# Kernel tuning notes

Hardware: AMD Instinct MI355X
Metric: run time of the kernel (lower is better)

The kernel has to match this reference:

```python
import jax, jax.numpy as jnp
import numpy as np

N_NODES = 100000
N_EDGES = 1600000
D_FEAT = 48


def sage_conv(x, src, dst, Wl, Wr, b):
    # mean aggregation of neighbor messages x[src] at dst (PyG source_to_target)
    msg_sum = jax.ops.segment_sum(x[src], dst, num_segments=N_NODES)  # [N, d]
    cnt = jax.ops.segment_sum(jnp.ones((src.shape[0],), x.dtype), dst,
                              num_segments=N_NODES)  # [N]
    mean = msg_sum / jnp.maximum(cnt, 1.0)[:, None]
    # out = lin_l(mean neighbors) + lin_r(self); bias only on lin_l (PyG default)
    return mean @ Wl + b + x @ Wr


def setup_inputs() -> dict:
    key = jax.random.key(0)
    ks = jax.random.split(key, 8)
    x = jax.random.normal(ks[0], (N_NODES, D_FEAT), jnp.float32)
    edge_index = jax.random.randint(ks[1], (2, N_EDGES), 0, N_NODES, jnp.int64)
    def w(k, fi, fo):
        return jax.random.normal(k, (fi, fo), jnp.float32) / np.sqrt(fi)
    return {
        "x": x,
        "edge_index": edge_index,
        "W1l": w(ks[2], D_FEAT, 32), "W1r": w(ks[3], D_FEAT, 32),
        "b1": jnp.zeros((32,), jnp.float32),
        "W2l": w(ks[4], 32, 16), "W2r": w(ks[5], 32, 16),
        "b2": jnp.zeros((16,), jnp.float32),
        "Wlin": w(ks[6], 16, 2), "blin": jnp.zeros((2,), jnp.float32),
    }


def reference(x, edge_index, W1l, W1r, b1, W2l, W2r, b2, Wlin, blin):
    src, dst = edge_index[0], edge_index[1]
    h = jax.nn.relu(sage_conv(x, src, dst, W1l, W1r, b1))
    h = jax.nn.relu(sage_conv(h, src, dst, W2l, W2r, b2))
    return h @ Wlin + blin  # [N, 2] logits
```

## Files before the change

kernel.cpp:

```cpp
#include <hip/hip_runtime.h>
#include <hip/hip_bf16.h>


constexpr int NN  = 100000;
constexpr int NE  = 1600000;
constexpr int NCH = (NN + 255) / 256;
constexpr int NB  = 391;
constexpr int CAP = 4608;
constexpr int SEG = CAP + 3 * 256;
constexpr int T1  = 2048;
constexpr int NB1 = (NE + T1 - 1) / T1;

__device__ __forceinline__ float bl(unsigned u) { return __uint_as_float(u << 16); }
__device__ __forceinline__ float bh(unsigned u) { return __uint_as_float(u & 0xffff0000u); }
__device__ __forceinline__ unsigned f2b(float x) {
    unsigned u = __float_as_uint(x);
    return (u + 0x7fffu + ((u >> 16) & 1u)) >> 16;
}
__device__ __forceinline__ unsigned pack2(float a, float b) {
    return f2b(a) | (f2b(b) << 16);
}

__device__ __forceinline__ int wave_incl_scan(int v, int lane) {
#pragma unroll
    for (int d = 1; d < 64; d <<= 1) {
        int t = __shfl_up(v, d, 64);
        if (lane >= d) v += t;
    }
    return v;
}

__global__ __launch_bounds__(256) void k1_kernel(
    const float* __restrict__ X,
    const float* __restrict__ Wl,
    const float* __restrict__ Wr,
    const int*   __restrict__ ei,
    int* __restrict__ bsize, unsigned* __restrict__ bbuf,
    __hip_bfloat16* __restrict__ P, __hip_bfloat16* __restrict__ R)
{
    __shared__ float sW[2][48 * 32];
    __shared__ int hist[NB], base[NB];
    __shared__ int s_any;

    if (blockIdx.x < NCH) {
        for (int i = threadIdx.x; i < 48 * 32; i += 256) {
            sW[0][i] = Wl[i];
            sW[1][i] = Wr[i];
        }
        __syncthreads();
        int n = blockIdx.x * 256 + threadIdx.x;
        if (n > NN) return;
        if (n == NN) {
            uint4 z = make_uint4(0, 0, 0, 0);
            uint4* pp = reinterpret_cast<uint4*>(P + (size_t)NN * 32);
#pragma unroll
            for (int i = 0; i < 4; ++i) pp[i] = z;
            return;
        }
        float xr[48];
        const float4* xp = reinterpret_cast<const float4*>(X + (size_t)n * 48);
#pragma unroll
        for (int i = 0; i < 12; ++i) {
            float4 u = xp[i];
            xr[i*4+0] = u.x; xr[i*4+1] = u.y; xr[i*4+2] = u.z; xr[i*4+3] = u.w;
        }
        float accp[32], accr[32];
#pragma unroll
        for (int j = 0; j < 32; ++j) { accp[j] = 0.f; accr[j] = 0.f; }
#pragma unroll
        for (int k = 0; k < 48; ++k) {
            float xk = xr[k];
#pragma unroll
            for (int j = 0; j < 32; ++j) {
                accp[j] += xk * sW[0][k * 32 + j];
                accr[j] += xk * sW[1][k * 32 + j];
            }
        }
        uint4* pp = reinterpret_cast<uint4*>(P + (size_t)n * 32);
        uint4* rp = reinterpret_cast<uint4*>(R + (size_t)n * 32);
#pragma unroll
        for (int i = 0; i < 4; ++i) {
            uint4 u, v;
            u.x = pack2(accp[i*8+0], accp[i*8+1]); u.y = pack2(accp[i*8+2], accp[i*8+3]);
            u.z = pack2(accp[i*8+4], accp[i*8+5]); u.w = pack2(accp[i*8+6], accp[i*8+7]);
            v.x = pack2(accr[i*8+0], accr[i*8+1]); v.y = pack2(accr[i*8+2], accr[i*8+3]);
            v.z = pack2(accr[i*8+4], accr[i*8+5]); v.w = pack2(accr[i*8+6], accr[i*8+7]);
            pp[i] = u;
            rp[i] = v;
        }
    } else {
        if (threadIdx.x == 0) s_any = 0;
        for (int i = threadIdx.x; i < NB; i += 256) hist[i] = 0;
        __syncthreads();
        int dv = 0;
        for (int i = threadIdx.x; i < 2048; i += 256) dv |= ei[2 * i + 1];
        if (dv != 0) atomicOr(&s_any, 1);
        __syncthreads();
        const bool i64 = (s_any == 0);
        const int e0 = (blockIdx.x - NCH) * T1;

        auto sweep = [&](auto&& f) {
            if (i64) {
                const int4* sp = reinterpret_cast<const int4*>(ei) + (e0 >> 1);
                const int4* dp = reinterpret_cast<const int4*>(ei) + ((NE + e0) >> 1);
#pragma unroll
                for (int it = 0; it < 4; ++it) {
                    int p = it * 256 + threadIdx.x;
                    int e = e0 + 2 * p;
                    if (e + 2 <= NE) {
                        int4 s4 = sp[p], d4 = dp[p];
                        f(s4.x, d4.x);
                        f(s4.z, d4.z);
                    } else {
                        for (int e2 = e; e2 < NE && e2 < e + 2; ++e2)
                            f(ei[(size_t)e2 << 1], ei[(size_t)(NE + e2) << 1]);
                    }
                }
            } else {
                const int4* sp = reinterpret_cast<const int4*>(ei) + (e0 >> 2);
                const int4* dp = reinterpret_cast<const int4*>(ei) + ((NE + e0) >> 2);
#pragma unroll
                for (int it = 0; it < 2; ++it) {
                    int q = it * 256 + threadIdx.x;
                    int e = e0 + 4 * q;
                    if (e + 4 <= NE) {
                        int4 s4 = sp[q], d4 = dp[q];
                        f(s4.x, d4.x);
                        f(s4.y, d4.y);
                        f(s4.z, d4.z);
                        f(s4.w, d4.w);
                    } else {
                        for (int e2 = e; e2 < NE && e2 < e + 4; ++e2)
                            f(ei[e2], ei[NE + e2]);
                    }
                }
            }
        };

        sweep([&](int s, int d) {
            if ((unsigned)s < (unsigned)NN && (unsigned)d < (unsigned)NN)
                atomicAdd(&hist[d >> 8], 1);
        });
        __syncthreads();
        for (int b = threadIdx.x; b < NB; b += 256) {
            int h = hist[b];
            base[b] = h ? atomicAdd(&bsize[b], h) : 0;
        }
        __syncthreads();
        sweep([&](int s, int d) {
            if ((unsigned)s < (unsigned)NN && (unsigned)d < (unsigned)NN) {
                int bk = d >> 8;
                int pos = atomicAdd(&base[bk], 1);
                if (pos < CAP)
                    bbuf[(size_t)bk * CAP + pos] =
                        ((unsigned)s << 8) | (unsigned)(d & 255);
            }
        });
    }
}

__global__ __launch_bounds__(1024) void k2_kernel(
    const int* __restrict__ bsize, const unsigned* __restrict__ bbuf,
    int* __restrict__ deg, int* __restrict__ rowstart, int* __restrict__ csr_src)
{
    __shared__ int ldeg[256], lcur[256], ws[4];
    int b = blockIdx.x, t = threadIdx.x;
    int bs = b * SEG;

    int S = min(bsize[b], CAP);
    const unsigned* bp = bbuf + (size_t)b * CAP;
    if (t < 256) ldeg[t] = 0;
    __syncthreads();
    for (int i = t; i < S; i += 1024)
        atomicAdd(&ldeg[bp[i] & 255u], 1);
    __syncthreads();

    int v = 0, pv = 0, incl = 0, excl = 0;
    if (t < 256) {
        v  = ldeg[t];
        pv = (v + 3) & ~3;
        incl = wave_incl_scan(pv, t & 63);
        if ((t & 63) == 63) ws[t >> 6] = incl;
    }
    __syncthreads();
    if (t < 256) {
        int off = 0, wid = t >> 6;
#pragma unroll
        for (int w = 0; w < 3; ++w)
            if (wid > w) off += ws[w];
        excl = off + incl - pv;
        int node = (b << 8) + t;
        if (node < NN) {
            deg[node] = v;
            rowstart[node] = bs + excl;
        }
        lcur[t] = excl;
    }
    __syncthreads();

    for (int i = t; i < S; i += 1024) {
        unsigned pk = bp[i];
        int pos = atomicAdd(&lcur[pk & 255u], 1);
        csr_src[bs + pos] = (int)(pk >> 8);
    }
    if (t < 256)
        for (int p = excl + v; p < excl + pv; ++p)
            csr_src[bs + p] = NN;
}

__global__ __launch_bounds__(256) void gather1f_kernel(
    const int* __restrict__ rowstart, const int* __restrict__ deg,
    const int* __restrict__ csr_src,
    const __hip_bfloat16* __restrict__ p1,
    const __hip_bfloat16* __restrict__ r1,
    const float* __restrict__ b1,
    const float* __restrict__ W2l,
    const float* __restrict__ W2r,
    __hip_bfloat16* __restrict__ P2,
    __hip_bfloat16* __restrict__ R2)
{
    __shared__ float sW2l[32 * 16], sW2r[32 * 16], sb1[32];
    __shared__ float shh[32 * 65];
    int t = threadIdx.x;
    for (int i = t; i < 32 * 16; i += 256) { sW2l[i] = W2l[i]; sW2r[i] = W2r[i]; }
    if (t < 32) sb1[t] = b1[t];
    __syncthreads();

    int loc = t >> 2, c = t & 3;
    int n = blockIdx.x * 64 + loc;
    bool valid = n < NN;

    if (valid) {
        int start = rowstart[n], dn = deg[n];
        int pv4 = ((dn + 3) & ~3) >> 2;
        const uint4* prow = reinterpret_cast<const uint4*>(p1);
        const int4* cp4 = reinterpret_cast<const int4*>(csr_src + start);
        uint4 r = reinterpret_cast<const uint4*>(r1)[(size_t)n * 4 + c];
        float acc[8];
#pragma unroll
        for (int j = 0; j < 8; ++j) acc[j] = 0.f;
        int4 s4 = cp4[0];
        for (int k = 0; k < pv4; ++k) {
            int4 nx = cp4[k + 1];
            uint4 a = prow[(size_t)s4.x * 4 + c];
            uint4 b = prow[(size_t)s4.y * 4 + c];
            uint4 d = prow[(size_t)s4.z * 4 + c];
            uint4 e = prow[(size_t)s4.w * 4 + c];
            acc[0] += bl(a.x) + bl(b.x) + bl(d.x) + bl(e.x);
            acc[1] += bh(a.x) + bh(b.x) + bh(d.x) + bh(e.x);
            acc[2] += bl(a.y) + bl(b.y) + bl(d.y) + bl(e.y);
            acc[3] += bh(a.y) + bh(b.y) + bh(d.y) + bh(e.y);
            acc[4] += bl(a.z) + bl(b.z) + bl(d.z) + bl(e.z);
            acc[5] += bh(a.z) + bh(b.z) + bh(d.z) + bh(e.z);
            acc[6] += bl(a.w) + bl(b.w) + bl(d.w) + bl(e.w);
            acc[7] += bh(a.w) + bh(b.w) + bh(d.w) + bh(e.w);
            s4 = nx;
        }
        float inv = 1.0f / fmaxf((float)dn, 1.0f);
        float rr[8] = { bl(r.x), bh(r.x), bl(r.y), bh(r.y),
                        bl(r.z), bh(r.z), bl(r.w), bh(r.w) };
#pragma unroll
        for (int j = 0; j < 8; ++j)
            shh[(c * 8 + j) * 65 + loc] = fmaxf(acc[j] * inv + rr[j] + sb1[c * 8 + j], 0.f);
    }
    __syncthreads();

    if (valid) {
        float accp[4], accr[4];
#pragma unroll
        for (int j = 0; j < 4; ++j) { accp[j] = 0.f; accr[j] = 0.f; }
#pragma unroll
        for (int k = 0; k < 32; ++k) {
            float hk = shh[k * 65 + loc];
#pragma unroll
            for (int j = 0; j < 4; ++j) {
                accp[j] += hk * sW2l[k * 16 + c * 4 + j];
                accr[j] += hk * sW2r[k * 16 + c * 4 + j];
            }
        }
        uint2 up, ur;
        up.x = pack2(accp[0], accp[1]); up.y = pack2(accp[2], accp[3]);
        ur.x = pack2(accr[0], accr[1]); ur.y = pack2(accr[2], accr[3]);
        reinterpret_cast<uint2*>(P2)[(size_t)n * 4 + c] = up;
        reinterpret_cast<uint2*>(R2)[(size_t)n * 4 + c] = ur;
    } else if (n == NN) {
        uint2 z = make_uint2(0, 0);
        reinterpret_cast<uint2*>(P2)[(size_t)NN * 4 + c] = z;
        reinterpret_cast<uint2*>(R2)[(size_t)NN * 4 + c] = z;
    }
}

__global__ __launch_bounds__(256) void gather2_kernel(
    const int* __restrict__ rowstart, const int* __restrict__ deg,
    const int* __restrict__ csr_src,
    const __hip_bfloat16* __restrict__ P2,
    const __hip_bfloat16* __restrict__ R2,
    const float* __restrict__ b2,
    const float* __restrict__ Wlin,
    const float* __restrict__ blin,
    float* __restrict__ out)
{
    __shared__ float sb[16], sW[32], sbl[2];
    if (threadIdx.x < 16) sb[threadIdx.x] = b2[threadIdx.x];
    else if (threadIdx.x < 48) sW[threadIdx.x - 16] = Wlin[threadIdx.x - 16];
    else if (threadIdx.x < 50) sbl[threadIdx.x - 48] = blin[threadIdx.x - 48];
    __syncthreads();
    int t = blockIdx.x * 256 + threadIdx.x;
    int n = t >> 1, c = t & 1;
    if (n >= NN) return;
    int start = rowstart[n], dn = deg[n];
    int pv4 = ((dn + 3) & ~3) >> 2;

    const uint4* prow = reinterpret_cast<const uint4*>(P2);
    const int4* cp4 = reinterpret_cast<const int4*>(csr_src + start);
    uint4 r = reinterpret_cast<const uint4*>(R2)[(size_t)n * 2 + c];
    float acc[8];
#pragma unroll
    for (int j = 0; j < 8; ++j) acc[j] = 0.f;
    int4 s4 = cp4[0];
    for (int k = 0; k < pv4; ++k) {
        int4 nx = cp4[k + 1];
        uint4 a = prow[(size_t)s4.x * 2 + c];
        uint4 b = prow[(size_t)s4.y * 2 + c];
        uint4 d = prow[(size_t)s4.z * 2 + c];
        uint4 e = prow[(size_t)s4.w * 2 + c];
        acc[0] += bl(a.x) + bl(b.x) + bl(d.x) + bl(e.x);
        acc[1] += bh(a.x) + bh(b.x) + bh(d.x) + bh(e.x);
        acc[2] += bl(a.y) + bl(b.y) + bl(d.y) + bl(e.y);
        acc[3] += bh(a.y) + bh(b.y) + bh(d.y) + bh(e.y);
        acc[4] += bl(a.z) + bl(b.z) + bl(d.z) + bl(e.z);
        acc[5] += bh(a.z) + bh(b.z) + bh(d.z) + bh(e.z);
        acc[6] += bl(a.w) + bl(b.w) + bl(d.w) + bl(e.w);
        acc[7] += bh(a.w) + bh(b.w) + bh(d.w) + bh(e.w);
        s4 = nx;
    }
    float inv = 1.0f / fmaxf((float)dn, 1.0f);
    float rr[8] = { bl(r.x), bh(r.x), bl(r.y), bh(r.y),
                    bl(r.z), bh(r.z), bl(r.w), bh(r.w) };
    float o0 = 0.f, o1 = 0.f;
#pragma unroll
    for (int j = 0; j < 8; ++j) {
        int kk = c * 8 + j;
        float hv = fmaxf(acc[j] * inv + rr[j] + sb[kk], 0.f);
        o0 += hv * sW[kk * 2];
        o1 += hv * sW[kk * 2 + 1];
    }
    o0 += __shfl_xor(o0, 1, 64);
    o1 += __shfl_xor(o1, 1, 64);
    if (c == 0)
        reinterpret_cast<float2*>(out)[n] = make_float2(o0 + sbl[0], o1 + sbl[1]);
}

extern "C" void kernel_launch(void* const* d_in, const int* in_sizes, int n_in,
                              void* d_out, int out_size, void* d_ws, size_t ws_size,
                              hipStream_t stream)
{
    const float* x    = (const float*)d_in[0];
    const int*   ei   = (const int*)d_in[1];
    const float* W1l  = (const float*)d_in[2];
    const float* W1r  = (const float*)d_in[3];
    const float* b1   = (const float*)d_in[4];
    const float* W2l  = (const float*)d_in[5];
    const float* W2r  = (const float*)d_in[6];
    const float* b2   = (const float*)d_in[7];
    const float* Wlin = (const float*)d_in[8];
    const float* blin = (const float*)d_in[9];
    float* out = (float*)d_out;

    char* wsb = (char*)d_ws;
    int*      bsize    = (int*)(wsb + 64);
    int*      deg      = (int*)(wsb + 4096);
    int*      rowstart = (int*)(wsb + 404096);
    int*      csr_src  = (int*)(wsb + 804096);
    unsigned* bbuf     = (unsigned*)(wsb + 9300000);
    __hip_bfloat16* p1 = (__hip_bfloat16*)(wsb + 16600000);
    __hip_bfloat16* r1 = (__hip_bfloat16*)(wsb + 23100000);
    __hip_bfloat16* p2 = (__hip_bfloat16*)(wsb + 29600000);
    __hip_bfloat16* r2 = (__hip_bfloat16*)(wsb + 32900000);

    dim3 blk(256);

    hipMemsetAsync(bsize, 0, NB * sizeof(int), stream);
    k1_kernel<<<NCH + NB1, blk, 0, stream>>>(x, W1l, W1r, ei, bsize, bbuf, p1, r1);
    k2_kernel<<<NB, dim3(1024), 0, stream>>>(bsize, bbuf, deg, rowstart, csr_src);
    gather1f_kernel<<<(NN + 1 + 63) / 64, blk, 0, stream>>>(
        rowstart, deg, csr_src, p1, r1, b1, W2l, W2r, p2, r2);
    gather2_kernel<<<(NN * 2 + 255) / 256, blk, 0, stream>>>(
        rowstart, deg, csr_src, p2, r2, b2, Wlin, blin, out);
}
```

Before: 181.8 us.

## Replace CSR build and gathers with per-bucket LDS atomic scatter aggregation

Drops the CSR construction kernel and aggregates both layers directly from the destination-bucketed edge buffer. Each 1024-thread block owns 256 destination nodes and accumulates gathered bf16 neighbor rows into shared-memory float accumulators with LDS atomics, counting degrees the same way. This removes one kernel launch plus the csr_src/rowstart/deg global traffic, at the cost of heavy LDS atomic contention, only 391 blocks of parallelism, and a summation order that is no longer deterministic.

```diff
diff --git a/kernel.cpp b/kernel.cpp
--- a/kernel.cpp
+++ b/kernel.cpp
@@ -7,7 +7,6 @@
 constexpr int NCH = (NN + 255) / 256;
 constexpr int NB  = 391;
 constexpr int CAP = 4608;
-constexpr int SEG = CAP + 3 * 256;
 constexpr int T1  = 2048;
 constexpr int NB1 = (NE + T1 - 1) / T1;
 
@@ -19,15 +18,6 @@
 }
 __device__ __forceinline__ unsigned pack2(float a, float b) {
     return f2b(a) | (f2b(b) << 16);
-}
-
-__device__ __forceinline__ int wave_incl_scan(int v, int lane) {
-#pragma unroll
-    for (int d = 1; d < 64; d <<= 1) {
-        int t = __shfl_up(v, d, 64);
-        if (lane >= d) v += t;
-    }
-    return v;
 }
 
 __global__ __launch_bounds__(256) void k1_kernel(
@@ -159,58 +149,8 @@
     }
 }
 
-__global__ __launch_bounds__(1024) void k2_kernel(
+__global__ __launch_bounds__(1024) void eg1_kernel(
     const int* __restrict__ bsize, const unsigned* __restrict__ bbuf,
-    int* __restrict__ deg, int* __restrict__ rowstart, int* __restrict__ csr_src)
-{
-    __shared__ int ldeg[256], lcur[256], ws[4];
-    int b = blockIdx.x, t = threadIdx.x;
-    int bs = b * SEG;
-
-    int S = min(bsize[b], CAP);
-    const unsigned* bp = bbuf + (size_t)b * CAP;
-    if (t < 256) ldeg[t] = 0;
-    __syncthreads();
-    for (int i = t; i < S; i += 1024)
-        atomicAdd(&ldeg[bp[i] & 255u], 1);
-    __syncthreads();
-
-    int v = 0, pv = 0, incl = 0, excl = 0;
-    if (t < 256) {
-        v  = ldeg[t];
-        pv = (v + 3) & ~3;
-        incl = wave_incl_scan(pv, t & 63);
-        if ((t & 63) == 63) ws[t >> 6] = incl;
-    }
-    __syncthreads();
-    if (t < 256) {
-        int off = 0, wid = t >> 6;
-#pragma unroll
-        for (int w = 0; w < 3; ++w)
-            if (wid > w) off += ws[w];
-        excl = off + incl - pv;
-        int node = (b << 8) + t;
-        if (node < NN) {
-            deg[node] = v;
-            rowstart[node] = bs + excl;
-        }
-        lcur[t] = excl;
-    }
-    __syncthreads();
-
-    for (int i = t; i < S; i += 1024) {
-        unsigned pk = bp[i];
-        int pos = atomicAdd(&lcur[pk & 255u], 1);
-        csr_src[bs + pos] = (int)(pk >> 8);
-    }
-    if (t < 256)
-        for (int p = excl + v; p < excl + pv; ++p)
-            csr_src[bs + p] = NN;
-}
-
-__global__ __launch_bounds__(256) void gather1f_kernel(
-    const int* __restrict__ rowstart, const int* __restrict__ deg,
-    const int* __restrict__ csr_src,
     const __hip_bfloat16* __restrict__ p1,
     const __hip_bfloat16* __restrict__ r1,
     const float* __restrict__ b1,
@@ -219,59 +159,71 @@
     __hip_bfloat16* __restrict__ P2,
     __hip_bfloat16* __restrict__ R2)
 {
+    __shared__ float hacc[256 * 33];
+    __shared__ int ldeg[256];
     __shared__ float sW2l[32 * 16], sW2r[32 * 16], sb1[32];
-    __shared__ float shh[32 * 65];
-    int t = threadIdx.x;
-    for (int i = t; i < 32 * 16; i += 256) { sW2l[i] = W2l[i]; sW2r[i] = W2r[i]; }
-    if (t < 32) sb1[t] = b1[t];
-    __syncthreads();
-
-    int loc = t >> 2, c = t & 3;
-    int n = blockIdx.x * 64 + loc;
-    bool valid = n < NN;
-
-    if (valid) {
-        int start = rowstart[n], dn = deg[n];
-        int pv4 = ((dn + 3) & ~3) >> 2;
-        const uint4* prow = reinterpret_cast<const uint4*>(p1);
-        const int4* cp4 = reinterpret_cast<const int4*>(csr_src + start);
+
+    int t = threadIdx.x, b = blockIdx.x;
+    if (t < 512) { sW2l[t] = W2l[t]; sW2r[t] = W2r[t]; }
+    else if (t < 544) sb1[t - 512] = b1[t - 512];
+    for (int i = t; i < 256 * 33; i += 1024) hacc[i] = 0.f;
+    if (t < 256) ldeg[t] = 0;
+    __syncthreads();
+
+    int S = min(bsize[b], CAP);
+    const unsigned* bp = bbuf + (size_t)b * CAP;
+    const uint4* prow = reinterpret_cast<const uint4*>(p1);
+
+    int sub = t & 3, eb = t >> 2;
+    for (int i = eb; i < S; i += 512) {
+        unsigned pk0 = bp[i];
+        int i1 = i + 256;
+        bool has1 = i1 < S;
+        unsigned pk1 = has1 ? bp[i1] : 0u;
+        int s0 = (int)(pk0 >> 8), d0 = (int)(pk0 & 255u);
+        uint4 v0 = prow[(size_t)s0 * 4 + sub];
+        int s1 = (int)(pk1 >> 8), d1 = (int)(pk1 & 255u);
+        uint4 v1 = make_uint4(0, 0, 0, 0);
+        if (has1) v1 = prow[(size_t)s1 * 4 + sub];
+
+        float* h0 = &hacc[d0 * 33 + sub * 8];
+        atomicAdd(&h0[0], bl(v0.x)); atomicAdd(&h0[1], bh(v0.x));
+        atomicAdd(&h0[2], bl(v0.y)); atomicAdd(&h0[3], bh(v0.y));
+        atomicAdd(&h0[4], bl(v0.z)); atomicAdd(&h0[5], bh(v0.z));
+        atomicAdd(&h0[6], bl(v0.w)); atomicAdd(&h0[7], bh(v0.w));
+        if (sub == 0) atomicAdd(&ldeg[d0], 1);
+        if (has1) {
+            float* h1 = &hacc[d1 * 33 + sub * 8];
+            atomicAdd(&h1[0], bl(v1.x)); atomicAdd(&h1[1], bh(v1.x));
+            atomicAdd(&h1[2], bl(v1.y)); atomicAdd(&h1[3], bh(v1.y));
+            atomicAdd(&h1[4], bl(v1.z)); atomicAdd(&h1[5], bh(v1.z));
+            atomicAdd(&h1[6], bl(v1.w)); atomicAdd(&h1[7], bh(v1.w));
+            if (sub == 0) atomicAdd(&ldeg[d1], 1);
+        }
+    }
+    __syncthreads();
+
+    int ln = t >> 2, c = t & 3;
+    int n = (b << 8) + ln;
+    if (n < NN) {
+        float inv = 1.0f / fmaxf((float)ldeg[ln], 1.0f);
         uint4 r = reinterpret_cast<const uint4*>(r1)[(size_t)n * 4 + c];
-        float acc[8];
-#pragma unroll
-        for (int j = 0; j < 8; ++j) acc[j] = 0.f;
-        int4 s4 = cp4[0];
-        for (int k = 0; k < pv4; ++k) {
-            int4 nx = cp4[k + 1];
-            uint4 a = prow[(size_t)s4.x * 4 + c];
-            uint4 b = prow[(size_t)s4.y * 4 + c];
-            uint4 d = prow[(size_t)s4.z * 4 + c];
-            uint4 e = prow[(size_t)s4.w * 4 + c];
-            acc[0] += bl(a.x) + bl(b.x) + bl(d.x) + bl(e.x);
-            acc[1] += bh(a.x) + bh(b.x) + bh(d.x) + bh(e.x);
-            acc[2] += bl(a.y) + bl(b.y) + bl(d.y) + bl(e.y);
-            acc[3] += bh(a.y) + bh(b.y) + bh(d.y) + bh(e.y);
-            acc[4] += bl(a.z) + bl(b.z) + bl(d.z) + bl(e.z);
-            acc[5] += bh(a.z) + bh(b.z) + bh(d.z) + bh(e.z);
-            acc[6] += bl(a.w) + bl(b.w) + bl(d.w) + bl(e.w);
-            acc[7] += bh(a.w) + bh(b.w) + bh(d.w) + bh(e.w);
-            s4 = nx;
-        }
-        float inv = 1.0f / fmaxf((float)dn, 1.0f);
         float rr[8] = { bl(r.x), bh(r.x), bl(r.y), bh(r.y),
                         bl(r.z), bh(r.z), bl(r.w), bh(r.w) };
+        float* hd = &hacc[ln * 33 + c * 8];
 #pragma unroll
         for (int j = 0; j < 8; ++j)
-            shh[(c * 8 + j) * 65 + loc] = fmaxf(acc[j] * inv + rr[j] + sb1[c * 8 + j], 0.f);
-    }
-    __syncthreads();
-
-    if (valid) {
+            hd[j] = fmaxf(hd[j] * inv + rr[j] + sb1[c * 8 + j], 0.f);
+    }
+    __syncthreads();
+
+    if (n < NN) {
         float accp[4], accr[4];
 #pragma unroll
         for (int j = 0; j < 4; ++j) { accp[j] = 0.f; accr[j] = 0.f; }
 #pragma unroll
         for (int k = 0; k < 32; ++k) {
-            float hk = shh[k * 65 + loc];
+            float hk = hacc[ln * 33 + k];
 #pragma unroll
             for (int j = 0; j < 4; ++j) {
                 accp[j] += hk * sW2l[k * 16 + c * 4 + j];
@@ -283,16 +235,11 @@
         ur.x = pack2(accr[0], accr[1]); ur.y = pack2(accr[2], accr[3]);
         reinterpret_cast<uint2*>(P2)[(size_t)n * 4 + c] = up;
         reinterpret_cast<uint2*>(R2)[(size_t)n * 4 + c] = ur;
-    } else if (n == NN) {
-        uint2 z = make_uint2(0, 0);
-        reinterpret_cast<uint2*>(P2)[(size_t)NN * 4 + c] = z;
-        reinterpret_cast<uint2*>(R2)[(size_t)NN * 4 + c] = z;
-    }
-}
-
-__global__ __launch_bounds__(256) void gather2_kernel(
-    const int* __restrict__ rowstart, const int* __restrict__ deg,
-    const int* __restrict__ csr_src,
+    }
+}
+
+__global__ __launch_bounds__(1024) void eg2_kernel(
+    const int* __restrict__ bsize, const unsigned* __restrict__ bbuf,
     const __hip_bfloat16* __restrict__ P2,
     const __hip_bfloat16* __restrict__ R2,
     const float* __restrict__ b2,
@@ -300,53 +247,69 @@
     const float* __restrict__ blin,
     float* __restrict__ out)
 {
-    __shared__ float sb[16], sW[32], sbl[2];
-    if (threadIdx.x < 16) sb[threadIdx.x] = b2[threadIdx.x];
-    else if (threadIdx.x < 48) sW[threadIdx.x - 16] = Wlin[threadIdx.x - 16];
-    else if (threadIdx.x < 50) sbl[threadIdx.x - 48] = blin[threadIdx.x - 48];
-    __syncthreads();
-    int t = blockIdx.x * 256 + threadIdx.x;
-    int n = t >> 1, c = t & 1;
+    __shared__ float hacc[256 * 17];
+    __shared__ int ldeg[256];
+    __shared__ float sb2[16], sWl[32], sbl[2];
+
+    int t = threadIdx.x, b = blockIdx.x;
+    if (t < 16) sb2[t] = b2[t];
+    else if (t < 48) sWl[t - 16] = Wlin[t - 16];
+    else if (t < 50) sbl[t - 48] = blin[t - 48];
+    for (int i = t; i < 256 * 17; i += 1024) hacc[i] = 0.f;
+    if (t < 256) ldeg[t] = 0;
+    __syncthreads();
+
+    int S = min(bsize[b], CAP);
+    const unsigned* bp = bbuf + (size_t)b * CAP;
+    const uint4* prow = reinterpret_cast<const uint4*>(P2);
+
+    int sub = t & 1, eb = t >> 1;
+    for (int i = eb; i < S; i += 1024) {
+        unsigned pk0 = bp[i];
+        int i1 = i + 512;
+        bool has1 = i1 < S;
+        unsigned pk1 = has1 ? bp[i1] : 0u;
+        int s0 = (int)(pk0 >> 8), d0 = (int)(pk0 & 255u);
+        uint4 v0 = prow[(size_t)s0 * 2 + sub];
+        int s1 = (int)(pk1 >> 8), d1 = (int)(pk1 & 255u);
+        uint4 v1 = make_uint4(0, 0, 0, 0);
+        if (has1) v1 = prow[(size_t)s1 * 2 + sub];
+
+        float* h0 = &hacc[d0 * 17 + sub * 8];
+        atomicAdd(&h0[0], bl(v0.x)); atomicAdd(&h0[1], bh(v0.x));
+        atomicAdd(&h0[2], bl(v0.y)); atomicAdd(&h0[3], bh(v0.y));
+        atomicAdd(&h0[4], bl(v0.z)); atomicAdd(&h0[5], bh(v0.z));
+        atomicAdd(&h0[6], bl(v0.w)); atomicAdd(&h0[7], bh(v0.w));
+        if (sub == 0) atomicAdd(&ldeg[d0], 1);
+        if (has1) {
+            float* h1 = &hacc[d1 * 17 + sub * 8];
+            atomicAdd(&h1[0], bl(v1.x)); atomicAdd(&h1[1], bh(v1.x));
+            atomicAdd(&h1[2], bl(v1.y)); atomicAdd(&h1[3], bh(v1.y));
+            atomicAdd(&h1[4], bl(v1.z)); atomicAdd(&h1[5], bh(v1.z));
+            atomicAdd(&h1[6], bl(v1.w)); atomicAdd(&h1[7], bh(v1.w));
+            if (sub == 0) atomicAdd(&ldeg[d1], 1);
+        }
+    }
+    __syncthreads();
+
+    int ln = t >> 2, c = t & 3;
+    int n = (b << 8) + ln;
     if (n >= NN) return;
-    int start = rowstart[n], dn = deg[n];
-    int pv4 = ((dn + 3) & ~3) >> 2;
-
-    const uint4* prow = reinterpret_cast<const uint4*>(P2);
-    const int4* cp4 = reinterpret_cast<const int4*>(csr_src + start);
-    uint4 r = reinterpret_cast<const uint4*>(R2)[(size_t)n * 2 + c];
-    float acc[8];
-#pragma unroll
-    for (int j = 0; j < 8; ++j) acc[j] = 0.f;
-    int4 s4 = cp4[0];
-    for (int k = 0; k < pv4; ++k) {
-        int4 nx = cp4[k + 1];
-        uint4 a = prow[(size_t)s4.x * 2 + c];
-        uint4 b = prow[(size_t)s4.y * 2 + c];
-        uint4 d = prow[(size_t)s4.z * 2 + c];
-        uint4 e = prow[(size_t)s4.w * 2 + c];
-        acc[0] += bl(a.x) + bl(b.x) + bl(d.x) + bl(e.x);
-        acc[1] += bh(a.x) + bh(b.x) + bh(d.x) + bh(e.x);
-        acc[2] += bl(a.y) + bl(b.y) + bl(d.y) + bl(e.y);
-        acc[3] += bh(a.y) + bh(b.y) + bh(d.y) + bh(e.y);
-        acc[4] += bl(a.z) + bl(b.z) + bl(d.z) + bl(e.z);
-        acc[5] += bh(a.z) + bh(b.z) + bh(d.z) + bh(e.z);
-        acc[6] += bl(a.w) + bl(b.w) + bl(d.w) + bl(e.w);
-        acc[7] += bh(a.w) + bh(b.w) + bh(d.w) + bh(e.w);
-        s4 = nx;
-    }
-    float inv = 1.0f / fmaxf((float)dn, 1.0f);
-    float rr[8] = { bl(r.x), bh(r.x), bl(r.y), bh(r.y),
-                    bl(r.z), bh(r.z), bl(r.w), bh(r.w) };
+    float inv = 1.0f / fmaxf((float)ldeg[ln], 1.0f);
+    uint2 r = reinterpret_cast<const uint2*>(R2)[(size_t)n * 4 + c];
+    float rr[4] = { bl(r.x), bh(r.x), bl(r.y), bh(r.y) };
     float o0 = 0.f, o1 = 0.f;
 #pragma unroll
-    for (int j = 0; j < 8; ++j) {
-        int kk = c * 8 + j;
-        float hv = fmaxf(acc[j] * inv + rr[j] + sb[kk], 0.f);
-        o0 += hv * sW[kk * 2];
-        o1 += hv * sW[kk * 2 + 1];
+    for (int j = 0; j < 4; ++j) {
+        int kk = c * 4 + j;
+        float hv = fmaxf(hacc[ln * 17 + kk] * inv + rr[j] + sb2[kk], 0.f);
+        o0 += hv * sWl[kk * 2];
+        o1 += hv * sWl[kk * 2 + 1];
     }
     o0 += __shfl_xor(o0, 1, 64);
     o1 += __shfl_xor(o1, 1, 64);
+    o0 += __shfl_xor(o0, 2, 64);
+    o1 += __shfl_xor(o1, 2, 64);
     if (c == 0)
         reinterpret_cast<float2*>(out)[n] = make_float2(o0 + sbl[0], o1 + sbl[1]);
 }
@@ -369,22 +332,17 @@
 
     char* wsb = (char*)d_ws;
     int*      bsize    = (int*)(wsb + 64);
-    int*      deg      = (int*)(wsb + 4096);
-    int*      rowstart = (int*)(wsb + 404096);
-    int*      csr_src  = (int*)(wsb + 804096);
     unsigned* bbuf     = (unsigned*)(wsb + 9300000);
     __hip_bfloat16* p1 = (__hip_bfloat16*)(wsb + 16600000);
     __hip_bfloat16* r1 = (__hip_bfloat16*)(wsb + 23100000);
     __hip_bfloat16* p2 = (__hip_bfloat16*)(wsb + 29600000);
     __hip_bfloat16* r2 = (__hip_bfloat16*)(wsb + 32900000);
 
-    dim3 blk(256);
-
     hipMemsetAsync(bsize, 0, NB * sizeof(int), stream);
-    k1_kernel<<<NCH + NB1, blk, 0, stream>>>(x, W1l, W1r, ei, bsize, bbuf, p1, r1);
-    k2_kernel<<<NB, dim3(1024), 0, stream>>>(bsize, bbuf, deg, rowstart, csr_src);
-    gather1f_kernel<<<(NN + 1 + 63) / 64, blk, 0, stream>>>(
-        rowstart, deg, csr_src, p1, r1, b1, W2l, W2r, p2, r2);
-    gather2_kernel<<<(NN * 2 + 255) / 256, blk, 0, stream>>>(
-        rowstart, deg, csr_src, p2, r2, b2, Wlin, blin, out);
-}
+    k1_kernel<<<NCH + NB1, dim3(256), 0, stream>>>(
+        x, W1l, W1r, ei, bsize, bbuf, p1, r1);
+    eg1_kernel<<<NB, dim3(1024), 0, stream>>>(
+        bsize, bbuf, p1, r1, b1, W2l, W2r, p2, r2);
+    eg2_kernel<<<NB, dim3(1024), 0, stream>>>(
+        bsize, bbuf, p2, r2, b2, Wlin, blin, out);
+}
```

Result: slower. 646.4 us (+255.5%).
